# Performance work log

Measured on AMD Instinct MI355X. Metric: run time of the kernel, lower is better.

Reference implementation:

```python
import jax, jax.numpy as jnp
import numpy as np


def group_norm(x, g, b, groups, eps=1e-5):
    # x: (B, C, H, W), PyTorch GroupNorm semantics
    B, C, H, W = x.shape
    xr = x.reshape(B, groups, -1)
    m = xr.mean(-1, keepdims=True)
    v = xr.var(-1, keepdims=True)
    xn = ((xr - m) * jax.lax.rsqrt(v + eps)).reshape(B, C, H, W)
    return xn * g[:, None, None] + b[:, None, None]


def mamba(xs, in_w, conv_w, conv_b, xproj_w, dt_w, dt_b, A_log, D, out_w):
    # Standard Mamba block: in_proj -> causal depthwise conv -> SiLU ->
    # x_proj -> softplus(dt_proj) -> selective scan -> gate -> out_proj.
    Bsz, L, d = xs.shape
    di = in_w.shape[0] // 2
    r = dt_w.shape[1]
    n = A_log.shape[1]
    K = conv_w.shape[1]
    xz = xs @ in_w.T                           # (B, L, 2*di)
    xpart, z = xz[..., :di], xz[..., di:]
    xp = jnp.pad(xpart, ((0, 0), (K - 1, 0), (0, 0)))  # causal pad
    xc = conv_b + sum(xp[:, k:k + L, :] * conv_w[:, k] for k in range(K))
    xc = jax.nn.silu(xc)
    proj = xc @ xproj_w.T                      # (B, L, r + 2n)
    dt = proj[..., :r]
    Bm = proj[..., r:r + n]
    Cm = proj[..., r + n:]
    delta = jax.nn.softplus(dt @ dt_w.T + dt_b)   # (B, L, di)
    A = -jnp.exp(A_log)                            # (di, n)
    dA = jnp.exp(jnp.einsum('bld,dn->bldn', delta, A))
    dBu = jnp.einsum('bld,bln,bld->bldn', delta, Bm, xc)

    def step(h, inp):
        dA_t, dBu_t, C_t = inp
        h = dA_t * h + dBu_t                  # (B, di, n)
        return h, jnp.einsum('bdn,bn->bd', h, C_t)

    h0 = jnp.zeros((Bsz, di, n), xs.dtype)
    _, ys = jax.lax.scan(step, h0, (jnp.moveaxis(dA, 1, 0), jnp.moveaxis(dBu, 1, 0), jnp.moveaxis(Cm, 1, 0)))
    y = jnp.moveaxis(ys, 0, 1) + D * xc
    y = y * jax.nn.silu(z)
    return y @ out_w.T


def setup_inputs() -> dict:
    def nrm(i, shape, s=0.05):
        return jax.random.normal(jax.random.fold_in(jax.random.key(0), i), shape, dtype=jnp.float32) * s

    f32 = jnp.float32
    C = 128
    di, r, n = 256, 8, 16          # spa mamba: d_model=128, expand=2
    di2, r2 = 64, 2                # spe mamba: d_model=32
    A1 = jnp.log(jnp.broadcast_to(jnp.arange(1, n + 1, dtype=f32), (di, n)))
    A2 = jnp.log(jnp.broadcast_to(jnp.arange(1, n + 1, dtype=f32), (di2, n)))
    return {
        'x': nrm(0, (2, C, 64, 64), 1.0),
        'pe_w': nrm(1, (C, C)), 'pe_b': jnp.zeros((C,), f32),
        'pe_gn_g': jnp.ones((C,), f32), 'pe_gn_b': jnp.zeros((C,), f32),
        'spa_in_w': nrm(2, (2 * di, C)),
        'spa_conv_w': nrm(3, (di, 4)), 'spa_conv_b': jnp.zeros((di,), f32),
        'spa_xproj_w': nrm(4, (r + 2 * n, di)),
        'spa_dt_w': nrm(5, (di, r)), 'spa_dt_b': jnp.full((di,), -2.0, f32),
        'spa_Alog': A1, 'spa_D': jnp.ones((di,), f32),
        'spa_out_w': nrm(6, (C, di)),
        'spa_gn_g': jnp.ones((C,), f32), 'spa_gn_b': jnp.zeros((C,), f32),
        'spe_in_w': nrm(7, (2 * di2, 32)),
        'spe_conv_w': nrm(8, (di2, 4)), 'spe_conv_b': jnp.zeros((di2,), f32),
        'spe_xproj_w': nrm(9, (r2 + 2 * n, di2)),
        'spe_dt_w': nrm(10, (di2, r2)), 'spe_dt_b': jnp.full((di2,), -2.0, f32),
        'spe_Alog': A2, 'spe_D': jnp.ones((di2,), f32),
        'spe_out_w': nrm(11, (32, di2)),
        'spe_gn_g': jnp.ones((C,), f32), 'spe_gn_b': jnp.zeros((C,), f32),
        'fuse_w': jnp.full((2,), 0.5, f32),
        'cls_w': nrm(12, (10, C)), 'cls_b': jnp.zeros((10,), f32),
        'ref_dw_w': nrm(13, (C, 1, 3, 3)),
        'ref_gn_g': jnp.ones((C,), f32), 'ref_gn_b': jnp.zeros((C,), f32),
        'ref_pw_w': nrm(14, (1, C)), 'ref_pw_b': jnp.zeros((1,), f32),
        'alpha': jnp.asarray(1e-4, f32),
    }


def reference(x, pe_w, pe_b, pe_gn_g, pe_gn_b, spa_in_w, spa_conv_w, spa_conv_b, spa_xproj_w, spa_dt_w, spa_dt_b, spa_Alog, spa_D, spa_out_w, spa_gn_g, spa_gn_b, spe_in_w, spe_conv_w, spe_conv_b, spe_xproj_w, spe_dt_w, spe_dt_b, spe_Alog, spe_D, spe_out_w, spe_gn_g, spe_gn_b, fuse_w, cls_w, cls_b, ref_dw_w, ref_gn_g, ref_gn_b, ref_pw_w, ref_pw_b, alpha):
    B, _, H, W = x.shape
    # patch embedding: 1x1 conv + GroupNorm + SiLU
    h1 = jnp.einsum('bchw,oc->bohw', x, pe_w) + pe_b[:, None, None]
    h1 = jax.nn.silu(group_norm(h1, pe_gn_g, pe_gn_b, 4))
    # SpaMamba: scan over flattened spatial tokens (B, H*W, C)
    seq = h1.transpose(0, 2, 3, 1).reshape(B, H * W, -1)
    y = mamba(seq, spa_in_w, spa_conv_w, spa_conv_b, spa_xproj_w, spa_dt_w, spa_dt_b, spa_Alog, spa_D, spa_out_w)
    y = y.reshape(B, H, W, -1).transpose(0, 3, 1, 2)
    spa = jax.nn.silu(group_norm(y, spa_gn_g, spa_gn_b, 4)) + h1
    # SpeMamba: token_num=4, group_channel_num=32, channel_num=128 (no pad)
    seq2 = h1.transpose(0, 2, 3, 1).reshape(B * H * W, 4, 32)
    y2 = mamba(seq2, spe_in_w, spe_conv_w, spe_conv_b, spe_xproj_w, spe_dt_w, spe_dt_b, spe_Alog, spe_D, spe_out_w)
    y2 = y2.reshape(B, H, W, -1).transpose(0, 3, 1, 2)
    spe = h1 + jax.nn.silu(group_norm(y2, spe_gn_g, spe_gn_b, 4))
    # attention-weighted fusion + residual (BothMamba, use_att=True)
    wts = jax.nn.softmax(fuse_w)
    feat = spa * wts[0] + spe * wts[1] + h1
    # classifier head (1x1 conv)
    logits = jnp.einsum('bchw,oc->bohw', feat, cls_w) + cls_b[:, None, None]
    # BoundaryAwareLogitRefiner
    edge = jax.lax.conv_general_dilated(feat, ref_dw_w, (1, 1), ((1, 1), (1, 1)), feature_group_count=feat.shape[1], dimension_numbers=('NCHW', 'OIHW', 'NCHW'))
    edge = jax.nn.silu(group_norm(edge, ref_gn_g, ref_gn_b, 4))
    edge = jax.nn.sigmoid(jnp.einsum('bchw,oc->bohw', edge, ref_pw_w) + ref_pw_b[:, None, None])
    local = jax.lax.reduce_window(logits, 0.0, jax.lax.add, (1, 1, 3, 3), (1, 1, 1, 1), ((0, 0), (0, 0), (1, 1), (1, 1))) / 9.0  # count_include_pad=True
    return logits + alpha * (1.0 - edge) * (local - logits)
```

## Files before the change

kernel.cpp:

```cpp
#include <hip/hip_runtime.h>
#include <math.h>

#define DEV __device__ __forceinline__

DEV float sigm(float x){ return 1.f/(1.f+__expf(-x)); }
DEV float siluf(float x){ return x * sigm(x); }
DEV float softplusf(float x){ return x > 20.f ? x : log1pf(__expf(x)); }

static constexpr float NG = 131072.0f;
static constexpr float LOG2E = 1.4426950408889634f;

static constexpr size_t WS_H1    = 0;
static constexpr size_t WS_H1PRE = 1048576;
static constexpr size_t WS_XC    = 2097152;
static constexpr size_t WS_ZSIL  = 4194304;
static constexpr size_t WS_XZ    = 6291456;
static constexpr size_t WS_QOFF  = 6619136;
static constexpr size_t WS_LOG   = 8650752;
static constexpr size_t WS_Y     = 10485760;
static constexpr size_t WS_POFF  = 12582912;
static constexpr size_t WS_Y2    = 14155776;
static constexpr size_t WS_FEAT  = 15204352;
static constexpr size_t WS_STATS = 16252928;
static constexpr size_t WS_PEWT  = 16253056;
static constexpr size_t WS_INWT  = WS_PEWT  + 16384;
static constexpr size_t WS_OUTWT = WS_INWT  + 65536;

__global__ void __launch_bounds__(256)
k_red(const float* __restrict__ part, float* __restrict__ outS, int half){
  __shared__ float red[4];
  int b = blockIdx.x >> 3, j = blockIdx.x & 7;
  float s = 0.f;
  for (int i = b*half + threadIdx.x; i < (b+1)*half; i += 256)
    s += part[(size_t)i*8 + j];
  s += __shfl_xor(s,1); s += __shfl_xor(s,2); s += __shfl_xor(s,4);
  s += __shfl_xor(s,8); s += __shfl_xor(s,16); s += __shfl_xor(s,32);
  if ((threadIdx.x & 63) == 0) red[threadIdx.x>>6] = s;
  __syncthreads();
  if (threadIdx.x == 0) outS[b*8+j] = red[0]+red[1]+red[2]+red[3];
}

__global__ void __launch_bounds__(256)
k_transpose(const float* __restrict__ pe_w, const float* __restrict__ in_w,
            const float* __restrict__ out_w,
            float* __restrict__ peT, float* __restrict__ inT,
            float* __restrict__ outT){
  int i0 = blockIdx.x*256 + threadIdx.x;
  int nt = gridDim.x*256;
  for (int k = i0; k < 128*128; k += nt){ int r = k >> 7, c = k & 127; peT[c*128 + r] = pe_w[k]; }
  for (int k = i0; k < 512*128; k += nt){ int r = k >> 7, c = k & 127; inT[c*512 + r] = in_w[k]; }
  for (int k = i0; k < 128*256; k += nt){ int r = k >> 8, c = k & 255; outT[c*128 + r] = out_w[k]; }
}

__global__ void __launch_bounds__(256)
k_pe(const float* __restrict__ x, const float* __restrict__ peT,
     const float* __restrict__ pe_b, float* __restrict__ h1pre,
     float* __restrict__ part){
  __shared__ float As[16][36];
  __shared__ float Bs[16][64];
  __shared__ float red1[2][4], red2[2][4];
  int tid = threadIdx.x;
  int bx = blockIdx.x, by = blockIdx.y;
  int m0 = bx*32, n0 = by*64;
  int b = m0 >> 12, pl0 = m0 & 4095;
  int tx = tid & 15, ty = tid >> 4;
  float acc[2][4];
  #pragma unroll
  for (int i = 0; i < 2; i++)
    #pragma unroll
    for (int j = 0; j < 4; j++) acc[i][j] = 0.f;
  for (int k0 = 0; k0 < 128; k0 += 16){
    if (tid < 128){
      int k = tid >> 3, mm = (tid & 7)*4;
      float4 a = *(const float4*)(x + ((size_t)b*128 + k0+k)*4096 + pl0 + mm);
      *(float4*)&As[k][mm] = a;
    }
    {
      int k = tid >> 4, n = (tid & 15)*4;
      *(float4*)&Bs[k][n] = *(const float4*)(peT + (size_t)(k0+k)*128 + n0+n);
    }
    __syncthreads();
    #pragma unroll
    for (int k = 0; k < 16; k++){
      float2 av = *(const float2*)&As[k][ty*2];
      float4 bv = *(const float4*)&Bs[k][tx*4];
      acc[0][0] += av.x*bv.x; acc[0][1] += av.x*bv.y; acc[0][2] += av.x*bv.z; acc[0][3] += av.x*bv.w;
      acc[1][0] += av.y*bv.x; acc[1][1] += av.y*bv.y; acc[1][2] += av.y*bv.z; acc[1][3] += av.y*bv.w;
    }
    __syncthreads();
  }
  float4 bias = *(const float4*)(pe_b + n0 + tx*4);
  float s1 = 0.f, s2 = 0.f;
  #pragma unroll
  for (int i = 0; i < 2; i++){
    float4 st;
    st.x = acc[i][0]+bias.x; st.y = acc[i][1]+bias.y;
    st.z = acc[i][2]+bias.z; st.w = acc[i][3]+bias.w;
    s1 += st.x+st.y+st.z+st.w;
    s2 += st.x*st.x + st.y*st.y + st.z*st.z + st.w*st.w;
    *(float4*)(h1pre + (size_t)(m0 + ty*2 + i)*128 + n0 + tx*4) = st;
  }
  s1 += __shfl_xor(s1,1);  s2 += __shfl_xor(s2,1);
  s1 += __shfl_xor(s1,2);  s2 += __shfl_xor(s2,2);
  s1 += __shfl_xor(s1,4);  s2 += __shfl_xor(s2,4);
  s1 += __shfl_xor(s1,16); s2 += __shfl_xor(s2,16);
  s1 += __shfl_xor(s1,32); s2 += __shfl_xor(s2,32);
  int lane = tid & 63, w = tid >> 6;
  if ((lane & 55) == 0){
    int gl = (lane >> 3) & 1;
    red1[gl][w] = s1; red2[gl][w] = s2;
  }
  __syncthreads();
  if (tid < 8){
    int gg = tid >> 1, which = tid & 1;
    int gl = gg - by*2;
    float v = 0.f;
    if (gl == 0 || gl == 1){
      v = which ? (red2[gl][0]+red2[gl][1]+red2[gl][2]+red2[gl][3])
                : (red1[gl][0]+red1[gl][1]+red1[gl][2]+red1[gl][3]);
    }
    int pblk = b*256 + (bx & 127) + by*128;
    part[(size_t)pblk*8 + tid] = v;
  }
}

__global__ void __launch_bounds__(256)
k_xz(const float* __restrict__ h1pre, const float* __restrict__ inT,
     const float* __restrict__ stats, const float* __restrict__ gng,
     const float* __restrict__ gnb, float* __restrict__ h1,
     float* __restrict__ xz, float* __restrict__ zsil){
  __shared__ float As[16][68];
  __shared__ float Bs[16][64];
  int tid = threadIdx.x;
  int m0 = blockIdx.x*64, n0 = blockIdx.y*64;
  int tx = tid & 15, ty = tid >> 4;
  float acc[4][4];
  #pragma unroll
  for (int i = 0; i < 4; i++)
    #pragma unroll
    for (int j = 0; j < 4; j++) acc[i][j] = 0.f;
  for (int k0 = 0; k0 < 128; k0 += 16){
    {
      int m = tid >> 2, kk = (tid & 3)*4;
      int pixm = m0 + m, c0 = k0 + kk;
      int bb = pixm >> 12, g = c0 >> 5;
      float4 a = *(const float4*)(h1pre + (size_t)pixm*128 + c0);
      float mu = stats[(bb*4+g)*2] * (1.f/NG);
      float var = stats[(bb*4+g)*2+1] * (1.f/NG) - mu*mu;
      float rs = rsqrtf(var + 1e-5f);
      float4 gg = *(const float4*)(gng + c0);
      float4 gb = *(const float4*)(gnb + c0);
      float4 v;
      v.x = siluf((a.x-mu)*rs*gg.x + gb.x);
      v.y = siluf((a.y-mu)*rs*gg.y + gb.y);
      v.z = siluf((a.z-mu)*rs*gg.z + gb.z);
      v.w = siluf((a.w-mu)*rs*gg.w + gb.w);
      As[kk+0][m] = v.x; As[kk+1][m] = v.y; As[kk+2][m] = v.z; As[kk+3][m] = v.w;
      if (blockIdx.y == 0) *(float4*)(h1 + (size_t)pixm*128 + c0) = v;
    }
    {
      int k = tid >> 4, n = (tid & 15)*4;
      *(float4*)&Bs[k][n] = *(const float4*)(inT + (size_t)(k0+k)*512 + n0+n);
    }
    __syncthreads();
    #pragma unroll
    for (int k = 0; k < 16; k++){
      float4 av = *(const float4*)&As[k][ty*4];
      float4 bv = *(const float4*)&Bs[k][tx*4];
      acc[0][0] += av.x*bv.x; acc[0][1] += av.x*bv.y; acc[0][2] += av.x*bv.z; acc[0][3] += av.x*bv.w;
      acc[1][0] += av.y*bv.x; acc[1][1] += av.y*bv.y; acc[1][2] += av.y*bv.z; acc[1][3] += av.y*bv.w;
      acc[2][0] += av.z*bv.x; acc[2][1] += av.z*bv.y; acc[2][2] += av.z*bv.z; acc[2][3] += av.z*bv.w;
      acc[3][0] += av.w*bv.x; acc[3][1] += av.w*bv.y; acc[3][2] += av.w*bv.z; acc[3][3] += av.w*bv.w;
    }
    __syncthreads();
  }
  if (n0 < 256){
    #pragma unroll
    for (int i = 0; i < 4; i++){
      float4 st; st.x = acc[i][0]; st.y = acc[i][1]; st.z = acc[i][2]; st.w = acc[i][3];
      *(float4*)(xz + (size_t)(m0 + ty*4 + i)*512 + n0 + tx*4) = st;
    }
  } else {
    #pragma unroll
    for (int i = 0; i < 4; i++){
      float4 st;
      st.x = siluf(acc[i][0]); st.y = siluf(acc[i][1]);
      st.z = siluf(acc[i][2]); st.w = siluf(acc[i][3]);
      *(float4*)(zsil + (size_t)(m0 + ty*4 + i)*256 + (n0-256) + tx*4) = st;
    }
  }
}

__global__ void __launch_bounds__(256)
k_conv(const float* __restrict__ xz, const float* __restrict__ cw,
       const float* __restrict__ cb, float* __restrict__ xc){
  int idx = blockIdx.x*256 + threadIdx.x;
  int d = idx & 255;
  int l = (idx >> 8) & 4095;
  int b = idx >> 20;
  float v = cb[d];
  #pragma unroll
  for (int k = 0; k < 4; k++){
    int ls = l - 3 + k;
    if (ls >= 0) v += xz[(size_t)(b*4096 + ls)*512 + d] * cw[d*4 + k];
  }
  xc[idx] = siluf(v);
}

__global__ void __launch_bounds__(256)
k_proj(const float* __restrict__ xc, const float* __restrict__ xpw,
       float* __restrict__ proj){
  __shared__ float As[32][33];
  int tid = threadIdx.x;
  int t = tid & 31;
  int jg = tid >> 5;
  int tok0 = blockIdx.x * 32;
  float acc[5];
  #pragma unroll
  for (int j = 0; j < 5; j++) acc[j] = 0.f;
  for (int k0 = 0; k0 < 256; k0 += 32){
    {
      int m = tid >> 3, kk = (tid & 7)*4;
      float4 a = *(const float4*)(xc + (size_t)(tok0+m)*256 + k0+kk);
      As[kk+0][m]=a.x; As[kk+1][m]=a.y; As[kk+2][m]=a.z; As[kk+3][m]=a.w;
    }
    __syncthreads();
    #pragma unroll
    for (int k4 = 0; k4 < 8; k4++){
      float a0 = As[k4*4+0][t];
      float a1 = As[k4*4+1][t];
      float a2 = As[k4*4+2][t];
      float a3 = As[k4*4+3][t];
      #pragma unroll
      for (int j = 0; j < 5; j++){
        float4 w = *(const float4*)(xpw + (size_t)(jg*5+j)*256 + k0 + k4*4);
        acc[j] += a0*w.x + a1*w.y + a2*w.z + a3*w.w;
      }
    }
    __syncthreads();
  }
  float* pr = proj + (size_t)(tok0+t)*40 + jg*5;
  #pragma unroll
  for (int j = 0; j < 5; j++) pr[j] = acc[j];
}

__global__ void __launch_bounds__(256)
k_delta(const float* __restrict__ proj, const float* __restrict__ dtw,
        const float* __restrict__ dtb, float* __restrict__ delta){
  int tid = threadIdx.x;
  int tok = blockIdx.x*4 + (tid >> 6);
  int lane = tid & 63;
  int d0 = lane*4;
  const float4* pr4 = (const float4*)(proj + (size_t)tok*40);
  float4 p0 = pr4[0], p1 = pr4[1];
  float4 outv;
  float* po = (float*)&outv;
  #pragma unroll
  for (int j = 0; j < 4; j++){
    int d = d0 + j;
    const float4* wr = (const float4*)(dtw + (size_t)d*8);
    float4 w0 = wr[0], w1 = wr[1];
    float v = dtb[d] + p0.x*w0.x + p0.y*w0.y + p0.z*w0.z + p0.w*w0.w
                     + p1.x*w1.x + p1.y*w1.y + p1.z*w1.z + p1.w*w1.w;
    po[j] = softplusf(v);
  }
  *(float4*)(delta + (size_t)tok*256 + d0) = outv;
}

__global__ void __launch_bounds__(256)
k_scan1(const float* __restrict__ delta, const float* __restrict__ proj,
        const float* __restrict__ xc, const float* __restrict__ Alog,
        float* __restrict__ P, float* __restrict__ Q){
  int blk = blockIdx.x;
  int dblk = blk & 3;
  int bc = blk >> 2;
  int b = bc >> 8, chunk = bc & 255;
  int tid = threadIdx.x;
  int dl = tid >> 2, ng = tid & 3;
  int d = dblk*64 + dl;
  float4 a4 = *(const float4*)(Alog + (size_t)d*16 + ng*4);
  float An[4] = {-__expf(a4.x)*LOG2E, -__expf(a4.y)*LOG2E,
                 -__expf(a4.z)*LOG2E, -__expf(a4.w)*LOG2E};
  float Pv[4] = {1.f,1.f,1.f,1.f}, Qv[4] = {0.f,0.f,0.f,0.f};
  size_t row0 = (size_t)(b*4096 + chunk*16);
  for (int l = 0; l < 16; l++){
    size_t r = row0 + l;
    float dv = delta[r*256 + d];
    float xv = xc[r*256 + d];
    float4 bm = *(const float4*)(proj + r*40 + 8 + ng*4);
    float dBx = dv*xv;
    float bmv[4] = {bm.x, bm.y, bm.z, bm.w};
    #pragma unroll
    for (int k = 0; k < 4; k++){
      float a = exp2f(dv*An[k]);
      Qv[k] = a*Qv[k] + bmv[k]*dBx;
      Pv[k] *= a;
    }
  }
  size_t o = (size_t)bc*4096 + dblk*1024 + tid*4;
  float4 pv; pv.x=Pv[0]; pv.y=Pv[1]; pv.z=Pv[2]; pv.w=Pv[3];
  float4 qv; qv.x=Qv[0]; qv.y=Qv[1]; qv.z=Qv[2]; qv.w=Qv[3];
  *(float4*)(P + o) = pv;
  *(float4*)(Q + o) = qv;
}

__global__ void __launch_bounds__(256)
k_scan2(const float* __restrict__ P, const float* __restrict__ Q,
        float* __restrict__ hs){
  __shared__ float Ps[256][17], Qs[256][17];
  int tid = threadIdx.x;
  int b = blockIdx.x >> 8;
  int dn0 = (blockIdx.x & 255) * 16;
  for (int i = tid; i < 1024; i += 256){
    int ch = i >> 2, g = (i & 3)*4;
    size_t gaddr = (size_t)(b*256+ch)*4096 + dn0 + g;
    float4 p = *(const float4*)(P + gaddr);
    float4 q = *(const float4*)(Q + gaddr);
    Ps[ch][g]=p.x; Ps[ch][g+1]=p.y; Ps[ch][g+2]=p.z; Ps[ch][g+3]=p.w;
    Qs[ch][g]=q.x; Qs[ch][g+1]=q.y; Qs[ch][g+2]=q.z; Qs[ch][g+3]=q.w;
  }
  __syncthreads();
  int lane = tid & 63, wv = tid >> 6;
  for (int rep = 0; rep < 4; rep++){
    int c = wv*4 + rep;
    float p0 = Ps[4*lane+0][c], q0 = Qs[4*lane+0][c];
    float p1 = Ps[4*lane+1][c], q1 = Qs[4*lane+1][c];
    float p2 = Ps[4*lane+2][c], q2 = Qs[4*lane+2][c];
    float p3 = Ps[4*lane+3][c], q3 = Qs[4*lane+3][c];
    float p = p0, q = q0;
    q = p1*q + q1; p *= p1;
    q = p2*q + q2; p *= p2;
    q = p3*q + q3; p *= p3;
    #pragma unroll
    for (int off = 1; off < 64; off <<= 1){
      float pp = __shfl_up(p, off);
      float qp = __shfl_up(q, off);
      if (lane >= off){ q = p*qp + q; p = p*pp; }
    }
    float h0 = __shfl_up(q, 1);
    if (lane == 0) h0 = 0.f;
    float h1 = p0*h0 + q0;
    float h2 = p1*h1 + q1;
    float h3 = p2*h2 + q2;
    Ps[4*lane+0][c] = h0;
    Ps[4*lane+1][c] = h1;
    Ps[4*lane+2][c] = h2;
    Ps[4*lane+3][c] = h3;
  }
  __syncthreads();
  for (int i = tid; i < 1024; i += 256){
    int ch = i >> 2, g = (i & 3)*4;
    size_t gaddr = (size_t)(b*256+ch)*4096 + dn0 + g;
    float4 h;
    h.x = Ps[ch][g]; h.y = Ps[ch][g+1]; h.z = Ps[ch][g+2]; h.w = Ps[ch][g+3];
    *(float4*)(hs + gaddr) = h;
  }
}

__global__ void __launch_bounds__(256)
k_scan3(const float* __restrict__ delta, const float* __restrict__ proj,
        const float* __restrict__ xc, const float* __restrict__ zsil,
        const float* __restrict__ Alog, const float* __restrict__ Dv,
        const float* __restrict__ hs, float* __restrict__ y){
  int blk = blockIdx.x;
  int dblk = blk & 3;
  int bc = blk >> 2;
  int b = bc >> 8, chunk = bc & 255;
  int tid = threadIdx.x;
  int dl = tid >> 2, ng = tid & 3;
  int d = dblk*64 + dl;
  float4 a4 = *(const float4*)(Alog + (size_t)d*16 + ng*4);
  float An[4] = {-__expf(a4.x)*LOG2E, -__expf(a4.y)*LOG2E,
                 -__expf(a4.z)*LOG2E, -__expf(a4.w)*LOG2E};
  float Dd = Dv[d];
  float h[4];
  {
    size_t o = (size_t)bc*4096 + dblk*1024 + tid*4;
    float4 hv = *(const float4*)(hs + o);
    h[0]=hv.x; h[1]=hv.y; h[2]=hv.z; h[3]=hv.w;
  }
  size_t row0 = (size_t)(b*4096 + chunk*16);
  for (int l = 0; l < 16; l++){
    size_t r = row0 + l;
    float dv = delta[r*256 + d];
    float xv = xc[r*256 + d];
    float4 bm = *(const float4*)(proj + r*40 + 8 + ng*4);
    float4 cm = *(const float4*)(proj + r*40 + 24 + ng*4);
    float dBx = dv*xv;
    float bmv[4] = {bm.x, bm.y, bm.z, bm.w};
    float cmv[4] = {cm.x, cm.y, cm.z, cm.w};
    float ys = 0.f;
    #pragma unroll
    for (int k = 0; k < 4; k++){
      float a = exp2f(dv*An[k]);
      h[k] = a*h[k] + bmv[k]*dBx;
      ys += h[k]*cmv[k];
    }
    ys += __shfl_xor(ys, 1);
    ys += __shfl_xor(ys, 2);
    if (ng == 0){
      float zv = zsil[r*256 + d];
      y[r*256 + d] = (ys + Dd*xv) * zv;
    }
  }
}

__global__ void __launch_bounds__(256)
k_outproj(const float* __restrict__ y, const float* __restrict__ outT,
          float* __restrict__ yproj, float* __restrict__ part){
  __shared__ float As[16][36];
  __shared__ float Bs[16][64];
  __shared__ float red1[2][4], red2[2][4];
  int tid = threadIdx.x;
  int bx = blockIdx.x, by = blockIdx.y;
  int m0 = bx*32, n0 = by*64;
  int b = m0 >> 12;
  int tx = tid & 15, ty = tid >> 4;
  float acc[2][4];
  #pragma unroll
  for (int i = 0; i < 2; i++)
    #pragma unroll
    for (int j = 0; j < 4; j++) acc[i][j] = 0.f;
  for (int k0 = 0; k0 < 256; k0 += 16){
    if (tid < 128){
      int m = tid >> 2, kk = (tid & 3)*4;
      float4 a = *(const float4*)(y + (size_t)(m0+m)*256 + k0+kk);
      As[kk+0][m] = a.x; As[kk+1][m] = a.y; As[kk+2][m] = a.z; As[kk+3][m] = a.w;
    }
    {
      int k = tid >> 4, n = (tid & 15)*4;
      *(float4*)&Bs[k][n] = *(const float4*)(outT + (size_t)(k0+k)*128 + n0+n);
    }
    __syncthreads();
    #pragma unroll
    for (int k = 0; k < 16; k++){
      float2 av = *(const float2*)&As[k][ty*2];
      float4 bv = *(const float4*)&Bs[k][tx*4];
      acc[0][0] += av.x*bv.x; acc[0][1] += av.x*bv.y; acc[0][2] += av.x*bv.z; acc[0][3] += av.x*bv.w;
      acc[1][0] += av.y*bv.x; acc[1][1] += av.y*bv.y; acc[1][2] += av.y*bv.z; acc[1][3] += av.y*bv.w;
    }
    __syncthreads();
  }
  float s1 = 0.f, s2 = 0.f;
  #pragma unroll
  for (int i = 0; i < 2; i++){
    float4 st; st.x = acc[i][0]; st.y = acc[i][1]; st.z = acc[i][2]; st.w = acc[i][3];
    s1 += st.x+st.y+st.z+st.w;
    s2 += st.x*st.x + st.y*st.y + st.z*st.z + st.w*st.w;
    *(float4*)(yproj + (size_t)(m0 + ty*2 + i)*128 + n0 + tx*4) = st;
  }
  s1 += __shfl_xor(s1,1);  s2 += __shfl_xor(s2,1);
  s1 += __shfl_xor(s1,2);  s2 += __shfl_xor(s2,2);
  s1 += __shfl_xor(s1,4);  s2 += __shfl_xor(s2,4);
  s1 += __shfl_xor(s1,16); s2 += __shfl_xor(s2,16);
  s1 += __shfl_xor(s1,32); s2 += __shfl_xor(s2,32);
  int lane = tid & 63, w = tid >> 6;
  if ((lane & 55) == 0){
    int gl = (lane >> 3) & 1;
    red1[gl][w] = s1; red2[gl][w] = s2;
  }
  __syncthreads();
  if (tid < 8){
    int gg = tid >> 1, which = tid & 1;
    int gl = gg - by*2;
    float v = 0.f;
    if (gl == 0 || gl == 1){
      v = which ? (red2[gl][0]+red2[gl][1]+red2[gl][2]+red2[gl][3])
                : (red1[gl][0]+red1[gl][1]+red1[gl][2]+red1[gl][3]);
    }
    int pblk = b*256 + (bx & 127) + by*128;
    part[(size_t)pblk*8 + tid] = v;
  }
}

__global__ void __launch_bounds__(256)
k_spe_a(const float* __restrict__ h1, const float* __restrict__ in_w,
        const float* __restrict__ conv_w, const float* __restrict__ conv_b,
        float* __restrict__ xc2, float* __restrict__ xc2T,
        float* __restrict__ zsil2){
  __shared__ float s_in[4][128];
  int tid = threadIdx.x;
  int w = tid >> 6, lane = tid & 63;
  float wx[32], wz[32];
  {
    const float4* rx = (const float4*)(in_w + (size_t)lane*32);
    const float4* rz = (const float4*)(in_w + (size_t)(64+lane)*32);
    #pragma unroll
    for (int k = 0; k < 8; k++){
      float4 a = rx[k]; wx[k*4]=a.x; wx[k*4+1]=a.y; wx[k*4+2]=a.z; wx[k*4+3]=a.w;
      float4 b = rz[k]; wz[k*4]=b.x; wz[k*4+1]=b.y; wz[k*4+2]=b.z; wz[k*4+3]=b.w;
    }
  }
  float4 cwv = ((const float4*)conv_w)[lane];
  float cbv = conv_b[lane];
  for (int i = 0; i < 4; i++){
    int pix = blockIdx.x*16 + w*4 + i;
    float2 hv = ((const float2*)(h1 + (size_t)pix*128))[lane];
    s_in[w][2*lane] = hv.x; s_in[w][2*lane+1] = hv.y;
    float xpr[4], zs[4];
    #pragma unroll
    for (int l = 0; l < 4; l++){
      const float4* sv = (const float4*)&s_in[w][l*32];
      float ax = 0.f, az = 0.f;
      #pragma unroll
      for (int c4 = 0; c4 < 8; c4++){
        float4 v = sv[c4];
        ax += v.x*wx[c4*4] + v.y*wx[c4*4+1] + v.z*wx[c4*4+2] + v.w*wx[c4*4+3];
        az += v.x*wz[c4*4] + v.y*wz[c4*4+1] + v.z*wz[c4*4+2] + v.w*wz[c4*4+3];
      }
      xpr[l] = ax; zs[l] = siluf(az);
    }
    #pragma unroll
    for (int l = 0; l < 4; l++){
      float v = cbv;
      if (l >= 3) v += xpr[l-3]*cwv.x;
      if (l >= 2) v += xpr[l-2]*cwv.y;
      if (l >= 1) v += xpr[l-1]*cwv.z;
      v += xpr[l]*cwv.w;
      float sx = siluf(v);
      int tok = pix*4 + l;
      xc2 [(size_t)tok*64 + lane] = sx;
      xc2T[(size_t)lane*32768 + tok] = sx;
      zsil2[(size_t)tok*64 + lane] = zs[l];
    }
  }
}

__global__ void __launch_bounds__(256)
k_spe_b(const float* __restrict__ xc2T, const float* __restrict__ xpw,
        float* __restrict__ proj){
  int tok = blockIdx.x*256 + threadIdx.x;
  float xcv[64];
  #pragma unroll 64
  for (int dd = 0; dd < 64; dd++) xcv[dd] = xc2T[(size_t)dd*32768 + tok];
  float* pr = proj + (size_t)tok*36;
  #pragma unroll 2
  for (int j = 0; j < 34; j++){
    const float4* wr = (const float4*)(xpw + j*64);
    float a = 0.f;
    #pragma unroll
    for (int k = 0; k < 16; k++){
      float4 wv = wr[k];
      a += xcv[k*4]*wv.x + xcv[k*4+1]*wv.y + xcv[k*4+2]*wv.z + xcv[k*4+3]*wv.w;
    }
    pr[j] = a;
  }
}

__global__ void __launch_bounds__(256)
k_spe_c(const float* __restrict__ xc2, const float* __restrict__ zsil2,
        const float* __restrict__ proj, const float* __restrict__ dt_w,
        const float* __restrict__ dt_b, const float* __restrict__ Alog,
        const float* __restrict__ Dvec, float* __restrict__ yg){
  int tid = threadIdx.x;
  int w = tid >> 6, lane = tid & 63;
  float2 dtwv = ((const float2*)dt_w)[lane];
  float dbv = dt_b[lane], Dd = Dvec[lane];
  float An[16];
  {
    const float4* ar = (const float4*)(Alog + (size_t)lane*16);
    #pragma unroll
    for (int k = 0; k < 4; k++){
      float4 a = ar[k];
      An[k*4]   = -__expf(a.x)*LOG2E; An[k*4+1] = -__expf(a.y)*LOG2E;
      An[k*4+2] = -__expf(a.z)*LOG2E; An[k*4+3] = -__expf(a.w)*LOG2E;
    }
  }
  for (int i = 0; i < 4; i++){
    int pix = blockIdx.x*16 + w*4 + i;
    float h[16];
    #pragma unroll
    for (int n = 0; n < 16; n++) h[n] = 0.f;
    #pragma unroll
    for (int l = 0; l < 4; l++){
      int tok = pix*4 + l;
      float pj[36];
      {
        const float4* pr = (const float4*)(proj + (size_t)tok*36);
        #pragma unroll
        for (int k = 0; k < 9; k++){
          float4 v = pr[k];
          pj[k*4]=v.x; pj[k*4+1]=v.y; pj[k*4+2]=v.z; pj[k*4+3]=v.w;
        }
      }
      float xv = xc2[(size_t)tok*64 + lane];
      float zv = zsil2[(size_t)tok*64 + lane];
      float dt = softplusf(dbv + pj[0]*dtwv.x + pj[1]*dtwv.y);
      float ys = 0.f;
      #pragma unroll
      for (int n = 0; n < 16; n++){
        float a = exp2f(dt * An[n]);
        h[n] = a*h[n] + dt * pj[2+n] * xv;
        ys += h[n] * pj[18+n];
      }
      yg[(size_t)tok*64 + lane] = (ys + Dd*xv) * zv;
    }
  }
}

__global__ void __launch_bounds__(256)
k_spe_d(const float* __restrict__ yg, const float* __restrict__ out_w,
        float* __restrict__ y2, float* __restrict__ part){
  __shared__ float ldsWT[64*32];
  __shared__ float bst[8];
  int tid = threadIdx.x;
  for (int i = tid; i < 2048; i += 256){
    int c2 = i >> 6, dd = i & 63;
    ldsWT[dd*32 + c2] = out_w[i];
  }
  if (tid < 8) bst[tid] = 0.f;
  __syncthreads();
  int w = tid >> 6, lane = tid & 63;
  int c2 = lane & 31, slot = lane >> 5;
  int tokbase = blockIdx.x*64 + w*16 + slot;
  float acc[8];
  #pragma unroll
  for (int i = 0; i < 8; i++) acc[i] = 0.f;
  for (int dd4 = 0; dd4 < 16; dd4++){
    float w0 = ldsWT[(dd4*4+0)*32 + c2];
    float w1 = ldsWT[(dd4*4+1)*32 + c2];
    float w2 = ldsWT[(dd4*4+2)*32 + c2];
    float w3 = ldsWT[(dd4*4+3)*32 + c2];
    #pragma unroll
    for (int i = 0; i < 8; i++){
      int tok = tokbase + 2*i;
      float4 yv = ((const float4*)(yg + (size_t)tok*64))[dd4];
      acc[i] += yv.x*w0 + yv.y*w1 + yv.z*w2 + yv.w*w3;
    }
  }
  #pragma unroll
  for (int i = 0; i < 8; i++){
    int tok = tokbase + 2*i;
    int pix = tok >> 2, l = tok & 3;
    y2[(size_t)pix*128 + l*32 + c2] = acc[i];
    float s1 = acc[i], s2 = acc[i]*acc[i];
    s1 += __shfl_xor(s1,1);  s2 += __shfl_xor(s2,1);
    s1 += __shfl_xor(s1,2);  s2 += __shfl_xor(s2,2);
    s1 += __shfl_xor(s1,4);  s2 += __shfl_xor(s2,4);
    s1 += __shfl_xor(s1,8);  s2 += __shfl_xor(s2,8);
    s1 += __shfl_xor(s1,16); s2 += __shfl_xor(s2,16);
    if (c2 == 0){
      atomicAdd(&bst[l*2+0], s1);
      atomicAdd(&bst[l*2+1], s2);
    }
  }
  __syncthreads();
  if (tid < 8) part[(size_t)blockIdx.x*8 + tid] = bst[tid];
}

__global__ void __launch_bounds__(256)
k_fuse(const float* __restrict__ h1, const float* __restrict__ yproj,
       const float* __restrict__ y2, const float* __restrict__ stats,
       const float* __restrict__ spa_g, const float* __restrict__ spa_b,
       const float* __restrict__ spe_g, const float* __restrict__ spe_b,
       const float* __restrict__ fuse_w, const float* __restrict__ cls_w,
       const float* __restrict__ cls_b, float* __restrict__ feat,
       float* __restrict__ logits){
  __shared__ float ft[2][128];
  int tid = threadIdx.x;
  int pixl = tid >> 7, c = tid & 127;
  int pix = blockIdx.x*2 + pixl;
  int b = pix >> 12, g = c >> 5;
  float m1 = stats[16 + (b*4+g)*2]   * (1.f/NG);
  float v1 = stats[16 + (b*4+g)*2+1] * (1.f/NG) - m1*m1;
  float m2 = stats[32 + (b*4+g)*2]   * (1.f/NG);
  float v2 = stats[32 + (b*4+g)*2+1] * (1.f/NG) - m2*m2;
  float h = h1[(size_t)pix*128 + c];
  float sa = siluf((yproj[(size_t)pix*128+c] - m1)*rsqrtf(v1+1e-5f)*spa_g[c] + spa_b[c]) + h;
  float sp = h + siluf((y2[(size_t)pix*128+c] - m2)*rsqrtf(v2+1e-5f)*spe_g[c] + spe_b[c]);
  float e0 = __expf(fuse_w[0]), e1 = __expf(fuse_w[1]);
  float w0 = e0/(e0+e1), w1 = e1/(e0+e1);
  float f = sa*w0 + sp*w1 + h;
  feat[(size_t)pix*128+c] = f;
  ft[pixl][c] = f;
  __syncthreads();
  if (tid < 20){
    int pl = (tid >= 10) ? 1 : 0;
    int o = tid - pl*10;
    float acc = cls_b[o];
    for (int cc = 0; cc < 128; cc++) acc += ft[pl][cc]*cls_w[o*128+cc];
    logits[(size_t)(blockIdx.x*2 + pl)*16 + o] = acc;
  }
}

__global__ void __launch_bounds__(256)
k_dw(const float* __restrict__ feat, const float* __restrict__ dww,
     float* __restrict__ epre, float* __restrict__ part){
  __shared__ float red1[4][64], red2[4][64];
  int tid = threadIdx.x;
  int pixl = tid >> 7, c = tid & 127;
  int pix = blockIdx.x*2 + pixl;
  int b = pix >> 12, p = pix & 4095, yy = p >> 6, xx = p & 63;
  float acc = 0.f;
  for (int dy = -1; dy <= 1; dy++){
    int ny = yy + dy; if (ny < 0 || ny > 63) continue;
    for (int dx = -1; dx <= 1; dx++){
      int nx = xx + dx; if (nx < 0 || nx > 63) continue;
      acc += feat[(size_t)((b<<12)|(ny<<6)|nx)*128 + c] * dww[c*9 + (dy+1)*3 + (dx+1)];
    }
  }
  epre[(size_t)pix*128 + c] = acc;
  int g = c >> 5;
  int idx = (c & 31) | (pixl << 5);
  red1[g][idx] = acc; red2[g][idx] = acc*acc;
  __syncthreads();
  int rg = tid >> 6, ridx = tid & 63;
  for (int s = 32; s >= 1; s >>= 1){
    if (ridx < s){ red1[rg][ridx] += red1[rg][ridx+s]; red2[rg][ridx] += red2[rg][ridx+s]; }
    __syncthreads();
  }
  if (ridx == 0){
    part[(size_t)blockIdx.x*8 + rg*2+0] = red1[rg][0];
    part[(size_t)blockIdx.x*8 + rg*2+1] = red2[rg][0];
  }
}

__global__ void __launch_bounds__(256)
k_final(const float* __restrict__ epre, const float* __restrict__ logits,
        const float* __restrict__ stats, const float* __restrict__ rg_g,
        const float* __restrict__ rg_b, const float* __restrict__ pw_w,
        const float* __restrict__ pw_b, const float* __restrict__ alpha,
        float* __restrict__ outp){
  __shared__ float part[4];
  __shared__ float edge_s[2];
  int tid = threadIdx.x;
  int pixl = tid >> 7, c = tid & 127;
  int pix = blockIdx.x*2 + pixl;
  int b = pix >> 12, p = pix & 4095, yy = p >> 6, xx = p & 63;
  int g = c >> 5;
  float m = stats[48 + (b*4+g)*2]   * (1.f/NG);
  float v = stats[48 + (b*4+g)*2+1] * (1.f/NG) - m*m;
  float e = epre[(size_t)pix*128+c];
  float en = siluf((e-m)*rsqrtf(v+1e-5f)*rg_g[c] + rg_b[c]);
  float pv = en * pw_w[c];
  pv += __shfl_xor(pv,1);  pv += __shfl_xor(pv,2);  pv += __shfl_xor(pv,4);
  pv += __shfl_xor(pv,8);  pv += __shfl_xor(pv,16); pv += __shfl_xor(pv,32);
  if ((tid & 63) == 0) part[tid>>6] = pv;
  __syncthreads();
  if (tid < 2) edge_s[tid] = sigm(part[tid*2] + part[tid*2+1] + pw_b[0]);
  __syncthreads();
  if (c < 10){
    float ed = edge_s[pixl];
    int o = c;
    float lg = logits[(size_t)pix*16 + o];
    float loc = 0.f;
    for (int dy = -1; dy <= 1; dy++){
      int ny = yy+dy; if (ny < 0 || ny > 63) continue;
      for (int dx = -1; dx <= 1; dx++){
        int nx = xx+dx; if (nx < 0 || nx > 63) continue;
        loc += logits[(size_t)((b<<12)|(ny<<6)|nx)*16 + o];
      }
    }
    loc *= (1.f/9.f);
    outp[(size_t)((b*10+o)<<12) + p] = lg + alpha[0]*(1.f-ed)*(loc - lg);
  }
}

extern "C" void kernel_launch(void* const* d_in, const int* in_sizes, int n_in,
                              void* d_out, int out_size, void* d_ws, size_t ws_size,
                              hipStream_t stream){
  const float* x          = (const float*)d_in[0];
  const float* pe_w       = (const float*)d_in[1];
  const float* pe_b       = (const float*)d_in[2];
  const float* pe_gn_g    = (const float*)d_in[3];
  const float* pe_gn_b    = (const float*)d_in[4];
  const float* spa_in_w   = (const float*)d_in[5];
  const float* spa_conv_w = (const float*)d_in[6];
  const float* spa_conv_b = (const float*)d_in[7];
  const float* spa_xproj_w= (const float*)d_in[8];
  const float* spa_dt_w   = (const float*)d_in[9];
  const float* spa_dt_b   = (const float*)d_in[10];
  const float* spa_Alog   = (const float*)d_in[11];
  const float* spa_D      = (const float*)d_in[12];
  const float* spa_out_w  = (const float*)d_in[13];
  const float* spa_gn_g   = (const float*)d_in[14];
  const float* spa_gn_b   = (const float*)d_in[15];
  const float* spe_in_w   = (const float*)d_in[16];
  const float* spe_conv_w = (const float*)d_in[17];
  const float* spe_conv_b = (const float*)d_in[18];
  const float* spe_xproj_w= (const float*)d_in[19];
  const float* spe_dt_w   = (const float*)d_in[20];
  const float* spe_dt_b   = (const float*)d_in[21];
  const float* spe_Alog   = (const float*)d_in[22];
  const float* spe_D      = (const float*)d_in[23];
  const float* spe_out_w  = (const float*)d_in[24];
  const float* spe_gn_g   = (const float*)d_in[25];
  const float* spe_gn_b   = (const float*)d_in[26];
  const float* fuse_w     = (const float*)d_in[27];
  const float* cls_w      = (const float*)d_in[28];
  const float* cls_b      = (const float*)d_in[29];
  const float* ref_dw_w   = (const float*)d_in[30];
  const float* ref_gn_g   = (const float*)d_in[31];
  const float* ref_gn_b   = (const float*)d_in[32];
  const float* ref_pw_w   = (const float*)d_in[33];
  const float* ref_pw_b   = (const float*)d_in[34];
  const float* alpha      = (const float*)d_in[35];
  float* ws  = (float*)d_ws;
  float* out = (float*)d_out;

  float* Pb    = ws + WS_POFF;
  float* Qb    = ws + WS_QOFF;
  float* HSb   = Pb;
  float* dely  = ws + WS_Y;
  float* partPE  = ws + WS_Y;
  float* partSPA = ws + WS_POFF;
  float* partSPE = ws + WS_POFF + 16384;
  float* partDW  = ws + WS_POFF + 65536;
  float* proj  = ws + WS_XZ;
  float* xc2   = ws + WS_XC;
  float* xc2T  = ws + WS_ZSIL;
  float* zsil2 = ws + WS_XZ;
  float* proj2 = ws + WS_XZ + 2097152;
  float* yg    = ws + WS_Y;

  k_transpose<<<64,256,0,stream>>>(pe_w, spa_in_w, spa_out_w,
      ws+WS_PEWT, ws+WS_INWT, ws+WS_OUTWT);
  k_pe<<<dim3(256,2),256,0,stream>>>(x, ws+WS_PEWT, pe_b, ws+WS_H1PRE, partPE);
  k_red<<<16,256,0,stream>>>(partPE, ws+WS_STATS+0, 256);
  k_xz<<<dim3(128,8),256,0,stream>>>(ws+WS_H1PRE, ws+WS_INWT, ws+WS_STATS,
      pe_gn_g, pe_gn_b, ws+WS_H1, ws+WS_XZ, ws+WS_ZSIL);
  k_conv<<<8192,256,0,stream>>>(ws+WS_XZ, spa_conv_w, spa_conv_b, ws+WS_XC);
  k_proj<<<256,256,0,stream>>>(ws+WS_XC, spa_xproj_w, proj);
  k_delta<<<2048,256,0,stream>>>(proj, spa_dt_w, spa_dt_b, dely);
  k_scan1<<<2048,256,0,stream>>>(dely, proj, ws+WS_XC, spa_Alog, Pb, Qb);
  k_scan2<<<512,256,0,stream>>>(Pb, Qb, HSb);
  k_scan3<<<2048,256,0,stream>>>(dely, proj, ws+WS_XC, ws+WS_ZSIL,
      spa_Alog, spa_D, HSb, dely );
  k_outproj<<<dim3(256,2),256,0,stream>>>(dely, ws+WS_OUTWT, ws+WS_H1PRE, partSPA);
  k_red<<<16,256,0,stream>>>(partSPA, ws+WS_STATS+16, 256);
  k_spe_a<<<512,256,0,stream>>>(ws+WS_H1, spe_in_w, spe_conv_w, spe_conv_b,
      xc2, xc2T, zsil2);
  k_spe_b<<<128,256,0,stream>>>(xc2T, spe_xproj_w, proj2);
  k_spe_c<<<512,256,0,stream>>>(xc2, zsil2, proj2, spe_dt_w, spe_dt_b,
      spe_Alog, spe_D, yg);
  k_spe_d<<<512,256,0,stream>>>(yg, spe_out_w, ws+WS_Y2, partSPE);
  k_red<<<16,256,0,stream>>>(partSPE, ws+WS_STATS+32, 256);
  k_fuse<<<4096,256,0,stream>>>(ws+WS_H1, ws+WS_H1PRE, ws+WS_Y2, ws+WS_STATS,
      spa_gn_g, spa_gn_b, spe_gn_g, spe_gn_b, fuse_w, cls_w, cls_b,
      ws+WS_FEAT, ws+WS_LOG);
  k_dw<<<4096,256,0,stream>>>(ws+WS_FEAT, ref_dw_w, ws+WS_Y, partDW);
  k_red<<<16,256,0,stream>>>(partDW, ws+WS_STATS+48, 2048);
  k_final<<<4096,256,0,stream>>>(ws+WS_Y, ws+WS_LOG, ws+WS_STATS,
      ref_gn_g, ref_gn_b, ref_pw_w, ref_pw_b, alpha, out);
  (void)in_sizes; (void)n_in; (void)out_size; (void)ws_size;
}
```

Baseline: 387.7 us.

## Fuse conv into x_proj, tile depthwise conv in LDS, drop weight transpose kernel

Removes the separate weight-transpose launch by loading untransposed weights and transposing them while staging into shared memory in the pe, in_proj and out_proj GEMMs, whose grids are also reordered. Fuses the causal depthwise conv and SiLU into the x_proj kernel so xc is taken from shared memory instead of being reread from global memory. Rewrites the 3x3 depthwise refiner conv to stage a haloed 8x8 tile in LDS and accumulate stats per thread over 32 pixels, using far fewer blocks. The dw kernel now launches only 128 blocks, which may underfill the GPU, and the proj buffer is moved to the FEAT region.

Result: no change. 384.1 us (-0.9%).

```diff
diff --git a/kernel.cpp b/kernel.cpp
--- a/kernel.cpp
+++ b/kernel.cpp
@@ -22,9 +22,6 @@
 static constexpr size_t WS_Y2    = 14155776;
 static constexpr size_t WS_FEAT  = 15204352;
 static constexpr size_t WS_STATS = 16252928;
-static constexpr size_t WS_PEWT  = 16253056;
-static constexpr size_t WS_INWT  = WS_PEWT  + 16384;
-static constexpr size_t WS_OUTWT = WS_INWT  + 65536;
 
 __global__ void __launch_bounds__(256)
 k_red(const float* __restrict__ part, float* __restrict__ outS, int half){
@@ -41,27 +38,15 @@
 }
 
 __global__ void __launch_bounds__(256)
-k_transpose(const float* __restrict__ pe_w, const float* __restrict__ in_w,
-            const float* __restrict__ out_w,
-            float* __restrict__ peT, float* __restrict__ inT,
-            float* __restrict__ outT){
-  int i0 = blockIdx.x*256 + threadIdx.x;
-  int nt = gridDim.x*256;
-  for (int k = i0; k < 128*128; k += nt){ int r = k >> 7, c = k & 127; peT[c*128 + r] = pe_w[k]; }
-  for (int k = i0; k < 512*128; k += nt){ int r = k >> 7, c = k & 127; inT[c*512 + r] = in_w[k]; }
-  for (int k = i0; k < 128*256; k += nt){ int r = k >> 8, c = k & 255; outT[c*128 + r] = out_w[k]; }
-}
-
-__global__ void __launch_bounds__(256)
-k_pe(const float* __restrict__ x, const float* __restrict__ peT,
+k_pe(const float* __restrict__ x, const float* __restrict__ pe_w,
      const float* __restrict__ pe_b, float* __restrict__ h1pre,
      float* __restrict__ part){
   __shared__ float As[16][36];
   __shared__ float Bs[16][64];
   __shared__ float red1[2][4], red2[2][4];
   int tid = threadIdx.x;
-  int bx = blockIdx.x, by = blockIdx.y;
-  int m0 = bx*32, n0 = by*64;
+  int nx = blockIdx.x, my = blockIdx.y;
+  int m0 = my*32, n0 = nx*64;
   int b = m0 >> 12, pl0 = m0 & 4095;
   int tx = tid & 15, ty = tid >> 4;
   float acc[2][4];
@@ -76,8 +61,9 @@
       *(float4*)&As[k][mm] = a;
     }
     {
-      int k = tid >> 4, n = (tid & 15)*4;
-      *(float4*)&Bs[k][n] = *(const float4*)(peT + (size_t)(k0+k)*128 + n0+n);
+      int n = tid >> 2, kq = (tid & 3)*4;
+      float4 a = *(const float4*)(pe_w + (size_t)(n0+n)*128 + k0 + kq);
+      Bs[kq+0][n] = a.x; Bs[kq+1][n] = a.y; Bs[kq+2][n] = a.z; Bs[kq+3][n] = a.w;
     }
     __syncthreads();
     #pragma unroll
@@ -113,26 +99,26 @@
   __syncthreads();
   if (tid < 8){
     int gg = tid >> 1, which = tid & 1;
-    int gl = gg - by*2;
+    int gl = gg - nx*2;
     float v = 0.f;
     if (gl == 0 || gl == 1){
       v = which ? (red2[gl][0]+red2[gl][1]+red2[gl][2]+red2[gl][3])
                 : (red1[gl][0]+red1[gl][1]+red1[gl][2]+red1[gl][3]);
     }
-    int pblk = b*256 + (bx & 127) + by*128;
+    int pblk = b*256 + (my & 127)*2 + nx;
     part[(size_t)pblk*8 + tid] = v;
   }
 }
 
 __global__ void __launch_bounds__(256)
-k_xz(const float* __restrict__ h1pre, const float* __restrict__ inT,
+k_xz(const float* __restrict__ h1pre, const float* __restrict__ in_w,
      const float* __restrict__ stats, const float* __restrict__ gng,
      const float* __restrict__ gnb, float* __restrict__ h1,
      float* __restrict__ xz, float* __restrict__ zsil){
   __shared__ float As[16][68];
   __shared__ float Bs[16][64];
   int tid = threadIdx.x;
-  int m0 = blockIdx.x*64, n0 = blockIdx.y*64;
+  int m0 = blockIdx.y*64, n0 = blockIdx.x*64;
   int tx = tid & 15, ty = tid >> 4;
   float acc[4][4];
   #pragma unroll
@@ -156,11 +142,12 @@
       v.z = siluf((a.z-mu)*rs*gg.z + gb.z);
       v.w = siluf((a.w-mu)*rs*gg.w + gb.w);
       As[kk+0][m] = v.x; As[kk+1][m] = v.y; As[kk+2][m] = v.z; As[kk+3][m] = v.w;
-      if (blockIdx.y == 0) *(float4*)(h1 + (size_t)pixm*128 + c0) = v;
+      if (blockIdx.x == 0) *(float4*)(h1 + (size_t)pixm*128 + c0) = v;
     }
     {
-      int k = tid >> 4, n = (tid & 15)*4;
-      *(float4*)&Bs[k][n] = *(const float4*)(inT + (size_t)(k0+k)*512 + n0+n);
+      int n = tid >> 2, kq = (tid & 3)*4;
+      float4 a = *(const float4*)(in_w + (size_t)(n0+n)*128 + k0 + kq);
+      Bs[kq+0][n] = a.x; Bs[kq+1][n] = a.y; Bs[kq+2][n] = a.z; Bs[kq+3][n] = a.w;
     }
     __syncthreads();
     #pragma unroll
@@ -192,56 +179,67 @@
 }
 
 __global__ void __launch_bounds__(256)
-k_conv(const float* __restrict__ xz, const float* __restrict__ cw,
-       const float* __restrict__ cb, float* __restrict__ xc){
-  int idx = blockIdx.x*256 + threadIdx.x;
-  int d = idx & 255;
-  int l = (idx >> 8) & 4095;
-  int b = idx >> 20;
-  float v = cb[d];
-  #pragma unroll
-  for (int k = 0; k < 4; k++){
-    int ls = l - 3 + k;
-    if (ls >= 0) v += xz[(size_t)(b*4096 + ls)*512 + d] * cw[d*4 + k];
-  }
-  xc[idx] = siluf(v);
-}
-
-__global__ void __launch_bounds__(256)
-k_proj(const float* __restrict__ xc, const float* __restrict__ xpw,
-       float* __restrict__ proj){
-  __shared__ float As[32][33];
-  int tid = threadIdx.x;
-  int t = tid & 31;
-  int jg = tid >> 5;
-  int tok0 = blockIdx.x * 32;
-  float acc[5];
-  #pragma unroll
-  for (int j = 0; j < 5; j++) acc[j] = 0.f;
-  for (int k0 = 0; k0 < 256; k0 += 32){
-    {
-      int m = tid >> 3, kk = (tid & 7)*4;
-      float4 a = *(const float4*)(xc + (size_t)(tok0+m)*256 + k0+kk);
-      As[kk+0][m]=a.x; As[kk+1][m]=a.y; As[kk+2][m]=a.z; As[kk+3][m]=a.w;
-    }
-    __syncthreads();
-    #pragma unroll
-    for (int k4 = 0; k4 < 8; k4++){
-      float a0 = As[k4*4+0][t];
-      float a1 = As[k4*4+1][t];
-      float a2 = As[k4*4+2][t];
-      float a3 = As[k4*4+3][t];
+k_projc(const float* __restrict__ xz, const float* __restrict__ cw,
+        const float* __restrict__ cb, const float* __restrict__ xpw,
+        float* __restrict__ xc, float* __restrict__ proj){
+  __shared__ float xct[16*260];
+  int tid = threadIdx.x;
+  int m0 = blockIdx.x * 16;
+  {
+    int slot = tid >> 6, lane = tid & 63;
+    int d4 = lane*4;
+    float4 cbv = *(const float4*)(cb + d4);
+    float4 cw0 = *(const float4*)(cw + (size_t)(d4+0)*4);
+    float4 cw1 = *(const float4*)(cw + (size_t)(d4+1)*4);
+    float4 cw2 = *(const float4*)(cw + (size_t)(d4+2)*4);
+    float4 cw3 = *(const float4*)(cw + (size_t)(d4+3)*4);
+    const float* c0p = (const float*)&cw0;
+    const float* c1p = (const float*)&cw1;
+    const float* c2p = (const float*)&cw2;
+    const float* c3p = (const float*)&cw3;
+    for (int i = 0; i < 4; i++){
+      int t = slot*4 + i;
+      int tok = m0 + t;
+      int l = tok & 4095;
+      float4 acc = cbv;
       #pragma unroll
-      for (int j = 0; j < 5; j++){
-        float4 w = *(const float4*)(xpw + (size_t)(jg*5+j)*256 + k0 + k4*4);
-        acc[j] += a0*w.x + a1*w.y + a2*w.z + a3*w.w;
+      for (int k = 0; k < 4; k++){
+        int ls = l - 3 + k;
+        if (ls >= 0){
+          float4 xv = *(const float4*)(xz + (size_t)(tok-3+k)*512 + d4);
+          acc.x += xv.x * c0p[k];
+          acc.y += xv.y * c1p[k];
+          acc.z += xv.z * c2p[k];
+          acc.w += xv.w * c3p[k];
+        }
       }
-    }
-    __syncthreads();
-  }
-  float* pr = proj + (size_t)(tok0+t)*40 + jg*5;
-  #pragma unroll
-  for (int j = 0; j < 5; j++) pr[j] = acc[j];
+      float4 s;
+      s.x = siluf(acc.x); s.y = siluf(acc.y); s.z = siluf(acc.z); s.w = siluf(acc.w);
+      *(float4*)&xct[t*260 + d4] = s;
+      *(float4*)(xc + (size_t)tok*256 + d4) = s;
+    }
+  }
+  __syncthreads();
+  {
+    int t = tid & 15, jq = tid >> 4;
+    int tok = m0 + t;
+    float a0 = 0.f, a1 = 0.f, a2 = 0.f;
+    for (int k0 = 0; k0 < 256; k0 += 4){
+      float4 av = *(const float4*)&xct[t*260 + k0];
+      float4 w0 = *(const float4*)(xpw + (size_t)jq*256 + k0);
+      float4 w1 = *(const float4*)(xpw + (size_t)(jq+16)*256 + k0);
+      a0 += av.x*w0.x + av.y*w0.y + av.z*w0.z + av.w*w0.w;
+      a1 += av.x*w1.x + av.y*w1.y + av.z*w1.z + av.w*w1.w;
+      if (jq < 8){
+        float4 w2 = *(const float4*)(xpw + (size_t)(jq+32)*256 + k0);
+        a2 += av.x*w2.x + av.y*w2.y + av.z*w2.z + av.w*w2.w;
+      }
+    }
+    float* pr = proj + (size_t)tok*40;
+    pr[jq] = a0;
+    pr[jq+16] = a1;
+    if (jq < 8) pr[jq+32] = a2;
+  }
 }
 
 __global__ void __launch_bounds__(256)
@@ -406,14 +404,14 @@
 }
 
 __global__ void __launch_bounds__(256)
-k_outproj(const float* __restrict__ y, const float* __restrict__ outT,
+k_outproj(const float* __restrict__ y, const float* __restrict__ out_w,
           float* __restrict__ yproj, float* __restrict__ part){
   __shared__ float As[16][36];
   __shared__ float Bs[16][64];
   __shared__ float red1[2][4], red2[2][4];
   int tid = threadIdx.x;
-  int bx = blockIdx.x, by = blockIdx.y;
-  int m0 = bx*32, n0 = by*64;
+  int nx = blockIdx.x, my = blockIdx.y;
+  int m0 = my*32, n0 = nx*64;
   int b = m0 >> 12;
   int tx = tid & 15, ty = tid >> 4;
   float acc[2][4];
@@ -428,8 +426,9 @@
       As[kk+0][m] = a.x; As[kk+1][m] = a.y; As[kk+2][m] = a.z; As[kk+3][m] = a.w;
     }
     {
-      int k = tid >> 4, n = (tid & 15)*4;
-      *(float4*)&Bs[k][n] = *(const float4*)(outT + (size_t)(k0+k)*128 + n0+n);
+      int n = tid >> 2, kq = (tid & 3)*4;
+      float4 a = *(const float4*)(out_w + (size_t)(n0+n)*256 + k0 + kq);
+      Bs[kq+0][n] = a.x; Bs[kq+1][n] = a.y; Bs[kq+2][n] = a.z; Bs[kq+3][n] = a.w;
     }
     __syncthreads();
     #pragma unroll
@@ -462,13 +461,13 @@
   __syncthreads();
   if (tid < 8){
     int gg = tid >> 1, which = tid & 1;
-    int gl = gg - by*2;
+    int gl = gg - nx*2;
     float v = 0.f;
     if (gl == 0 || gl == 1){
       v = which ? (red2[gl][0]+red2[gl][1]+red2[gl][2]+red2[gl][3])
                 : (red1[gl][0]+red1[gl][1]+red1[gl][2]+red1[gl][3]);
     }
-    int pblk = b*256 + (bx & 127) + by*128;
+    int pblk = b*256 + (my & 127)*2 + nx;
     part[(size_t)pblk*8 + tid] = v;
   }
 }
@@ -686,23 +685,41 @@
 __global__ void __launch_bounds__(256)
 k_dw(const float* __restrict__ feat, const float* __restrict__ dww,
      float* __restrict__ epre, float* __restrict__ part){
+  __shared__ float ft[100*128];
   __shared__ float red1[4][64], red2[4][64];
   int tid = threadIdx.x;
-  int pixl = tid >> 7, c = tid & 127;
-  int pix = blockIdx.x*2 + pixl;
-  int b = pix >> 12, p = pix & 4095, yy = p >> 6, xx = p & 63;
-  float acc = 0.f;
-  for (int dy = -1; dy <= 1; dy++){
-    int ny = yy + dy; if (ny < 0 || ny > 63) continue;
-    for (int dx = -1; dx <= 1; dx++){
-      int nx = xx + dx; if (nx < 0 || nx > 63) continue;
-      acc += feat[(size_t)((b<<12)|(ny<<6)|nx)*128 + c] * dww[c*9 + (dy+1)*3 + (dx+1)];
-    }
-  }
-  epre[(size_t)pix*128 + c] = acc;
+  int blk = blockIdx.x;
+  int b = blk >> 6, ty = (blk >> 3) & 7, tx = blk & 7;
+  for (int idx = tid; idx < 100*128; idx += 256){
+    int row = idx >> 7, c = idx & 127;
+    int r10 = row / 10, c10 = row - r10*10;
+    int ry = ty*8 + r10 - 1, rx = tx*8 + c10 - 1;
+    float v = 0.f;
+    if (ry >= 0 && ry < 64 && rx >= 0 && rx < 64)
+      v = feat[(size_t)((b<<12)|(ry<<6)|rx)*128 + c];
+    ft[idx] = v;
+  }
+  __syncthreads();
+  int c = tid & 127, pl = tid >> 7;
+  float w[9];
+  #pragma unroll
+  for (int k = 0; k < 9; k++) w[k] = dww[c*9+k];
+  float s1 = 0.f, s2 = 0.f;
+  for (int i = 0; i < 32; i++){
+    int pixl = i*2 + pl;
+    int py = pixl >> 3, px = pixl & 7;
+    float acc = 0.f;
+    #pragma unroll
+    for (int dy = 0; dy < 3; dy++)
+      #pragma unroll
+      for (int dx = 0; dx < 3; dx++)
+        acc += ft[((py+dy)*10 + (px+dx))*128 + c] * w[dy*3+dx];
+    epre[(size_t)((b<<12)|((ty*8+py)<<6)|(tx*8+px))*128 + c] = acc;
+    s1 += acc; s2 += acc*acc;
+  }
   int g = c >> 5;
-  int idx = (c & 31) | (pixl << 5);
-  red1[g][idx] = acc; red2[g][idx] = acc*acc;
+  int idx = (c & 31) | (pl << 5);
+  red1[g][idx] = s1; red2[g][idx] = s2;
   __syncthreads();
   int rg = tid >> 6, ridx = tid & 63;
   for (int s = 32; s >= 1; s >>= 1){
@@ -710,8 +727,8 @@
     __syncthreads();
   }
   if (ridx == 0){
-    part[(size_t)blockIdx.x*8 + rg*2+0] = red1[rg][0];
-    part[(size_t)blockIdx.x*8 + rg*2+1] = red2[rg][0];
+    part[(size_t)blk*8 + rg*2+0] = red1[rg][0];
+    part[(size_t)blk*8 + rg*2+1] = red2[rg][0];
   }
 }
 
@@ -806,27 +823,25 @@
   float* partSPA = ws + WS_POFF;
   float* partSPE = ws + WS_POFF + 16384;
   float* partDW  = ws + WS_POFF + 65536;
-  float* proj  = ws + WS_XZ;
+  float* proj  = ws + WS_FEAT;
   float* xc2   = ws + WS_XC;
   float* xc2T  = ws + WS_ZSIL;
   float* zsil2 = ws + WS_XZ;
   float* proj2 = ws + WS_XZ + 2097152;
   float* yg    = ws + WS_Y;
 
-  k_transpose<<<64,256,0,stream>>>(pe_w, spa_in_w, spa_out_w,
-      ws+WS_PEWT, ws+WS_INWT, ws+WS_OUTWT);
-  k_pe<<<dim3(256,2),256,0,stream>>>(x, ws+WS_PEWT, pe_b, ws+WS_H1PRE, partPE);
+  k_pe<<<dim3(2,256),256,0,stream>>>(x, pe_w, pe_b, ws+WS_H1PRE, partPE);
   k_red<<<16,256,0,stream>>>(partPE, ws+WS_STATS+0, 256);
-  k_xz<<<dim3(128,8),256,0,stream>>>(ws+WS_H1PRE, ws+WS_INWT, ws+WS_STATS,
+  k_xz<<<dim3(8,128),256,0,stream>>>(ws+WS_H1PRE, spa_in_w, ws+WS_STATS,
       pe_gn_g, pe_gn_b, ws+WS_H1, ws+WS_XZ, ws+WS_ZSIL);
-  k_conv<<<8192,256,0,stream>>>(ws+WS_XZ, spa_conv_w, spa_conv_b, ws+WS_XC);
-  k_proj<<<256,256,0,stream>>>(ws+WS_XC, spa_xproj_w, proj);
+  k_projc<<<512,256,0,stream>>>(ws+WS_XZ, spa_conv_w, spa_conv_b, spa_xproj_w,
+      ws+WS_XC, proj);
   k_delta<<<2048,256,0,stream>>>(proj, spa_dt_w, spa_dt_b, dely);
   k_scan1<<<2048,256,0,stream>>>(dely, proj, ws+WS_XC, spa_Alog, Pb, Qb);
   k_scan2<<<512,256,0,stream>>>(Pb, Qb, HSb);
   k_scan3<<<2048,256,0,stream>>>(dely, proj, ws+WS_XC, ws+WS_ZSIL,
-      spa_Alog, spa_D, HSb, dely );
-  k_outproj<<<dim3(256,2),256,0,stream>>>(dely, ws+WS_OUTWT, ws+WS_H1PRE, partSPA);
+      spa_Alog, spa_D, HSb, dely);
+  k_outproj<<<dim3(2,256),256,0,stream>>>(dely, spa_out_w, ws+WS_H1PRE, partSPA);
   k_red<<<16,256,0,stream>>>(partSPA, ws+WS_STATS+16, 256);
   k_spe_a<<<512,256,0,stream>>>(ws+WS_H1, spe_in_w, spe_conv_w, spe_conv_b,
       xc2, xc2T, zsil2);
@@ -838,8 +853,8 @@
   k_fuse<<<4096,256,0,stream>>>(ws+WS_H1, ws+WS_H1PRE, ws+WS_Y2, ws+WS_STATS,
       spa_gn_g, spa_gn_b, spe_gn_g, spe_gn_b, fuse_w, cls_w, cls_b,
       ws+WS_FEAT, ws+WS_LOG);
-  k_dw<<<4096,256,0,stream>>>(ws+WS_FEAT, ref_dw_w, ws+WS_Y, partDW);
-  k_red<<<16,256,0,stream>>>(partDW, ws+WS_STATS+48, 2048);
+  k_dw<<<128,256,0,stream>>>(ws+WS_FEAT, ref_dw_w, ws+WS_Y, partDW);
+  k_red<<<16,256,0,stream>>>(partDW, ws+WS_STATS+48, 64);
   k_final<<<4096,256,0,stream>>>(ws+WS_Y, ws+WS_LOG, ws+WS_STATS,
       ref_gn_g, ref_gn_b, ref_pw_w, ref_pw_b, alpha, out);
   (void)in_sizes; (void)n_in; (void)out_size; (void)ws_size;
```
